# Kernel optimization log

Hardware: AMD Instinct MI355X
Metric: run time of the kernel (lower is better)

Reference implementation:

```python
import jax, jax.numpy as jnp
import numpy as np


def setup_inputs() -> dict:
    key = jax.random.key(0)
    ks = jax.random.split(key, 8)
    B, H, W = 4, 512, 256
    return {
        "x1": jax.random.normal(ks[0], (B, H, W), dtype=jnp.float32),
        "x2": jax.random.normal(ks[1], (B, H, W), dtype=jnp.float32),
        "wq": jax.random.normal(ks[2], (2, 2), dtype=jnp.float32) * 0.5,
        "bq": jax.random.normal(ks[3], (2,), dtype=jnp.float32) * 0.1,
        "wk": jax.random.normal(ks[4], (2, 2), dtype=jnp.float32) * 0.5,
        "bk": jax.random.normal(ks[5], (2,), dtype=jnp.float32) * 0.1,
        "wv": jax.random.normal(ks[6], (2, 2), dtype=jnp.float32) * 0.5,
        "bv": jax.random.normal(ks[7], (2,), dtype=jnp.float32) * 0.1,
    }


def reference(x1, x2, wq, bq, wk, bk, wv, bv):
    # input: [B, 2, H, W]
    inp = jnp.stack((x1, x2), axis=1)

    def proj(w, b):  # 1x1 conv == channel matmul; -> [B, 2, H, W]
        return jnp.einsum('oi,bihw->bohw', w, inp) + b[None, :, None, None]

    q = proj(wq, bq).transpose(0, 2, 3, 1)  # [B, H, W, 2]
    k = proj(wk, bk).transpose(0, 2, 1, 3)  # [B, H, 2, W]
    v = proj(wv, bv).transpose(0, 2, 3, 1)  # [B, H, W, 2]

    qk = jnp.einsum('bhwc,bhcu->bhwu', q, k)  # [B, H, W, W]
    score = jax.nn.softmax(qk, axis=-1)
    out = jnp.einsum('bhwu,bhuc->bhwc', score, v)  # [B, H, W, 2]

    out1 = x1 + out[..., 0]
    out2 = x2 + out[..., 1]
    return (out1, out2)
```

## Files before the change

### kernel.cpp

```cpp
#include <hip/hip_runtime.h>

#define LOG2E 1.4426950408889634f

__device__ __forceinline__ float fast_exp2(float x) {
#if __has_builtin(__builtin_amdgcn_exp2f)
    return __builtin_amdgcn_exp2f(x);
#else
    return exp2f(x);
#endif
}

__global__ __launch_bounds__(256, 4) void csa_kernel(
    const float* __restrict__ x1, const float* __restrict__ x2,
    const float* __restrict__ wq, const float* __restrict__ bq,
    const float* __restrict__ wk, const float* __restrict__ bk,
    const float* __restrict__ wv, const float* __restrict__ bv,
    float* __restrict__ out1, float* __restrict__ out2)
{
    constexpr int W = 256;
    __shared__ float4 kv[W];
    __shared__ float redq[4], redk[4];

    const int tid = threadIdx.x;
    const long base = (long)blockIdx.x * W;

    const float xv1 = x1[base + tid];
    const float xv2 = x2[base + tid];

    const float wq00 = wq[0], wq01 = wq[1], wq10 = wq[2], wq11 = wq[3];
    const float wk00 = wk[0], wk01 = wk[1], wk10 = wk[2], wk11 = wk[3];
    const float wv00 = wv[0], wv01 = wv[1], wv10 = wv[2], wv11 = wv[3];
    const float bq0 = bq[0], bq1 = bq[1];
    const float bk0 = bk[0], bk1 = bk[1];
    const float bv0 = bv[0], bv1 = bv[1];

    const float q0 = fmaf(wq00, xv1, fmaf(wq01, xv2, bq0));
    const float q1 = fmaf(wq10, xv1, fmaf(wq11, xv2, bq1));
    const float k0 = fmaf(wk00, xv1, fmaf(wk01, xv2, bk0));
    const float k1 = fmaf(wk10, xv1, fmaf(wk11, xv2, bk1));
    const float v0 = fmaf(wv00, xv1, fmaf(wv01, xv2, bv0));
    const float v1 = fmaf(wv10, xv1, fmaf(wv11, xv2, bv1));

    kv[tid] = make_float4(k0, k1, v0, v1);

    float q2 = fmaf(q0, q0, q1 * q1);
    float k2 = fmaf(k0, k0, k1 * k1);
#pragma unroll
    for (int off = 32; off >= 1; off >>= 1) {
        q2 = fmaxf(q2, __shfl_xor(q2, off, 64));
        k2 = fmaxf(k2, __shfl_xor(k2, off, 64));
    }
    const int wave = tid >> 6;
    if ((tid & 63) == 0) { redq[wave] = q2; redk[wave] = k2; }
    __syncthreads();

    const float mq2 = fmaxf(fmaxf(redq[0], redq[1]), fmaxf(redq[2], redq[3]));
    const float mk2 = fmaxf(fmaxf(redk[0], redk[1]), fmaxf(redk[2], redk[3]));
    const float mb = sqrtf(mq2 * mk2);

    const float ql0 = q0 * LOG2E;
    const float ql1 = q1 * LOG2E;
    const float csh = -mb * LOG2E;

    float sum = 0.f, o0 = 0.f, o1 = 0.f;
#pragma unroll 8
    for (int u = 0; u < W; ++u) {
        const float4 t = kv[u];
        const float s = fmaf(ql0, t.x, fmaf(ql1, t.y, csh));
        const float e = fast_exp2(s);
        sum += e;
        o0 = fmaf(e, t.z, o0);
        o1 = fmaf(e, t.w, o1);
    }

    const float inv = 1.0f / sum;
    out1[base + tid] = fmaf(o0, inv, xv1);
    out2[base + tid] = fmaf(o1, inv, xv2);
}

extern "C" void kernel_launch(void* const* d_in, const int* in_sizes, int n_in,
                              void* d_out, int out_size, void* d_ws, size_t ws_size,
                              hipStream_t stream) {
    const float* x1 = (const float*)d_in[0];
    const float* x2 = (const float*)d_in[1];
    const float* wq = (const float*)d_in[2];
    const float* bq = (const float*)d_in[3];
    const float* wk = (const float*)d_in[4];
    const float* bk = (const float*)d_in[5];
    const float* wv = (const float*)d_in[6];
    const float* bv = (const float*)d_in[7];

    float* out = (float*)d_out;
    const int BHW = in_sizes[0];
    const int rows = BHW / 256;

    csa_kernel<<<rows, 256, 0, stream>>>(x1, x2, wq, bq, wk, bk, wv, bv,
                                         out, out + BHW);
}
```

Measured before the change: 92.09 us.

## Map one row per wavefront with four queries per lane and packed FMA

Each wavefront now handles a whole row, with every lane computing four query positions. Each K/V value read from LDS is reused across four queries, and the score and accumulate math uses packed 2-wide FMA. The cross-wave max reduction through shared memory goes away and loads and stores become float4. The cost is more registers per thread (launch bounds lowered to 2), a quarter as many blocks, and a leftover __syncthreads with an exponent shift bound now computed per row.

```diff
diff --git a/kernel.cpp b/kernel.cpp
--- a/kernel.cpp
+++ b/kernel.cpp
@@ -1,4 +1,6 @@
 #include <hip/hip_runtime.h>
+
+typedef float v2f __attribute__((ext_vector_type(2)));
 
 #define LOG2E 1.4426950408889634f
 
@@ -10,7 +12,11 @@
 #endif
 }
 
-__global__ __launch_bounds__(256, 4) void csa_kernel(
+__device__ __forceinline__ v2f pk_fma(v2f a, v2f b, v2f c) {
+    return __builtin_elementwise_fma(a, b, c);
+}
+
+__global__ __launch_bounds__(256, 2) void csa_kernel(
     const float* __restrict__ x1, const float* __restrict__ x2,
     const float* __restrict__ wq, const float* __restrict__ bq,
     const float* __restrict__ wk, const float* __restrict__ bk,
@@ -18,14 +24,19 @@
     float* __restrict__ out1, float* __restrict__ out2)
 {
     constexpr int W = 256;
-    __shared__ float4 kv[W];
-    __shared__ float redq[4], redk[4];
+    __shared__ float4 sK[4][W / 2];
+    __shared__ float4 sV[4][W / 2];
 
     const int tid = threadIdx.x;
-    const long base = (long)blockIdx.x * W;
+    const int wv_id = tid >> 6;
+    const int l = tid & 63;
+    const long row = (long)blockIdx.x * 4 + wv_id;
+    const long base = row * W;
 
-    const float xv1 = x1[base + tid];
-    const float xv2 = x2[base + tid];
+    const float4 xa = *(const float4*)(x1 + base + 4 * l);
+    const float4 xb = *(const float4*)(x2 + base + 4 * l);
+    const float X1[4] = {xa.x, xa.y, xa.z, xa.w};
+    const float X2[4] = {xb.x, xb.y, xb.z, xb.w};
 
     const float wq00 = wq[0], wq01 = wq[1], wq10 = wq[2], wq11 = wq[3];
     const float wk00 = wk[0], wk01 = wk[1], wk10 = wk[2], wk11 = wk[3];
@@ -34,48 +45,80 @@
     const float bk0 = bk[0], bk1 = bk[1];
     const float bv0 = bv[0], bv1 = bv[1];
 
-    const float q0 = fmaf(wq00, xv1, fmaf(wq01, xv2, bq0));
-    const float q1 = fmaf(wq10, xv1, fmaf(wq11, xv2, bq1));
-    const float k0 = fmaf(wk00, xv1, fmaf(wk01, xv2, bk0));
-    const float k1 = fmaf(wk10, xv1, fmaf(wk11, xv2, bk1));
-    const float v0 = fmaf(wv00, xv1, fmaf(wv01, xv2, bv0));
-    const float v1 = fmaf(wv10, xv1, fmaf(wv11, xv2, bv1));
+    float q0[4], q1[4], k0[4], k1[4], v0[4], v1[4];
+#pragma unroll
+    for (int j = 0; j < 4; ++j) {
+        q0[j] = fmaf(wq00, X1[j], fmaf(wq01, X2[j], bq0));
+        q1[j] = fmaf(wq10, X1[j], fmaf(wq11, X2[j], bq1));
+        k0[j] = fmaf(wk00, X1[j], fmaf(wk01, X2[j], bk0));
+        k1[j] = fmaf(wk10, X1[j], fmaf(wk11, X2[j], bk1));
+        v0[j] = fmaf(wv00, X1[j], fmaf(wv01, X2[j], bv0));
+        v1[j] = fmaf(wv10, X1[j], fmaf(wv11, X2[j], bv1));
+    }
 
-    kv[tid] = make_float4(k0, k1, v0, v1);
+    sK[wv_id][2 * l + 0] = make_float4(k0[0], k0[1], k1[0], k1[1]);
+    sK[wv_id][2 * l + 1] = make_float4(k0[2], k0[3], k1[2], k1[3]);
+    sV[wv_id][2 * l + 0] = make_float4(v0[0], v0[1], v1[0], v1[1]);
+    sV[wv_id][2 * l + 1] = make_float4(v0[2], v0[3], v1[2], v1[3]);
 
-    float q2 = fmaf(q0, q0, q1 * q1);
-    float k2 = fmaf(k0, k0, k1 * k1);
+    float q2 = 0.f, k2 = 0.f;
+#pragma unroll
+    for (int j = 0; j < 4; ++j) {
+        q2 = fmaxf(q2, fmaf(q0[j], q0[j], q1[j] * q1[j]));
+        k2 = fmaxf(k2, fmaf(k0[j], k0[j], k1[j] * k1[j]));
+    }
 #pragma unroll
     for (int off = 32; off >= 1; off >>= 1) {
         q2 = fmaxf(q2, __shfl_xor(q2, off, 64));
         k2 = fmaxf(k2, __shfl_xor(k2, off, 64));
     }
-    const int wave = tid >> 6;
-    if ((tid & 63) == 0) { redq[wave] = q2; redk[wave] = k2; }
+    const float mb = sqrtf(q2 * k2);
+    const float csh = -mb * LOG2E;
+
     __syncthreads();
 
-    const float mq2 = fmaxf(fmaxf(redq[0], redq[1]), fmaxf(redq[2], redq[3]));
-    const float mk2 = fmaxf(fmaxf(redk[0], redk[1]), fmaxf(redk[2], redk[3]));
-    const float mb = sqrtf(mq2 * mk2);
-
-    const float ql0 = q0 * LOG2E;
-    const float ql1 = q1 * LOG2E;
-    const float csh = -mb * LOG2E;
-
-    float sum = 0.f, o0 = 0.f, o1 = 0.f;
-#pragma unroll 8
-    for (int u = 0; u < W; ++u) {
-        const float4 t = kv[u];
-        const float s = fmaf(ql0, t.x, fmaf(ql1, t.y, csh));
-        const float e = fast_exp2(s);
-        sum += e;
-        o0 = fmaf(e, t.z, o0);
-        o1 = fmaf(e, t.w, o1);
+    const v2f cshv = {csh, csh};
+    v2f ql0[4], ql1[4], sum[4], o0[4], o1[4];
+#pragma unroll
+    for (int j = 0; j < 4; ++j) {
+        const float a0 = q0[j] * LOG2E, a1 = q1[j] * LOG2E;
+        ql0[j] = (v2f){a0, a0};
+        ql1[j] = (v2f){a1, a1};
+        sum[j] = (v2f){0.f, 0.f};
+        o0[j]  = (v2f){0.f, 0.f};
+        o1[j]  = (v2f){0.f, 0.f};
     }
 
-    const float inv = 1.0f / sum;
-    out1[base + tid] = fmaf(o0, inv, xv1);
-    out2[base + tid] = fmaf(o1, inv, xv2);
+#pragma unroll 4
+    for (int up = 0; up < W / 2; ++up) {
+        const float4 K = sK[wv_id][up];
+        const float4 V = sV[wv_id][up];
+        const v2f kx = {K.x, K.y};
+        const v2f kz = {K.z, K.w};
+        const v2f vx = {V.x, V.y};
+        const v2f vz = {V.z, V.w};
+#pragma unroll
+        for (int j = 0; j < 4; ++j) {
+            v2f s = pk_fma(ql0[j], kx, pk_fma(ql1[j], kz, cshv));
+            v2f e;
+            e.x = fast_exp2(s.x);
+            e.y = fast_exp2(s.y);
+            sum[j] += e;
+            o0[j] = pk_fma(e, vx, o0[j]);
+            o1[j] = pk_fma(e, vz, o1[j]);
+        }
+    }
+
+    float r1[4], r2[4];
+#pragma unroll
+    for (int j = 0; j < 4; ++j) {
+        const float s = sum[j].x + sum[j].y;
+        const float inv = 1.0f / s;
+        r1[j] = fmaf(o0[j].x + o0[j].y, inv, X1[j]);
+        r2[j] = fmaf(o1[j].x + o1[j].y, inv, X2[j]);
+    }
+    *(float4*)(out1 + base + 4 * l) = make_float4(r1[0], r1[1], r1[2], r1[3]);
+    *(float4*)(out2 + base + 4 * l) = make_float4(r2[0], r2[1], r2[2], r2[3]);
 }
 
 extern "C" void kernel_launch(void* const* d_in, const int* in_sizes, int n_in,
@@ -94,6 +137,6 @@
     const int BHW = in_sizes[0];
     const int rows = BHW / 256;
 
-    csa_kernel<<<rows, 256, 0, stream>>>(x1, x2, wq, bq, wk, bk, wv, bv,
-                                         out, out + BHW);
+    csa_kernel<<<rows / 4, 256, 0, stream>>>(x1, x2, wq, bq, wk, bk, wv, bv,
+                                             out, out + BHW);
 }
```

Result: no change. 91.63 us (-0.5%).
